# Optimization experiments

Measured on AMD Instinct MI355X. Metric: run time of the kernel, lower is better.

## Reference

```python
import jax, jax.numpy as jnp
import numpy as np
import math

N_EMBD = 2048
N_HEAD = 16
HEAD_DIM = N_EMBD // N_HEAD
EPS = 1e-6

def rms_norm(x, w):
    xf = x.astype(jnp.float32)
    n = xf * jax.lax.rsqrt(jnp.mean(xf * xf, axis=-1, keepdims=True) + EPS)
    return n.astype(x.dtype) * w

def rotate_embeddings(x):
    # pairs (a, b) -> (-b, a), interleaved on last dim
    x2 = x.reshape(*x.shape[:-1], -1, 2)
    rot = jnp.stack([-x2[..., 1], x2[..., 0]], axis=-1)
    return rot.reshape(x.shape)

def rope_angles(T, hd, dtype):
    # pos = 10000 ** ((-2*arange(0, hd, 2) - 1) / hd)  (faithful to source)
    i = jnp.arange(0, hd, 2, dtype=jnp.float32)
    pos = jnp.power(10000.0, (-2.0 * i - 1.0) / hd)
    token_seq = jnp.arange(T, dtype=jnp.float32)[:, None] * pos[None, :]  # [T, hd/2]
    ang = jnp.concatenate([token_seq, token_seq], axis=-1)  # [T, hd]
    return ang.astype(dtype)

def setup_inputs() -> dict:
    key = jax.random.key(0)
    k1, k2, k3 = jax.random.split(key, 3)
    B, T, C = 2, 2048, N_EMBD
    x = jax.random.normal(k1, (B, T, C), dtype=jnp.float32)
    s = 1.0 / math.sqrt(C)
    W_qkv = jax.random.normal(k2, (3 * C, C), dtype=jnp.float32) * s
    W_proj = jax.random.normal(k3, (C, C), dtype=jnp.float32) * s
    g_qk = jnp.ones((C,), dtype=jnp.float32)
    return {"x": x, "W_qkv": W_qkv, "W_proj": W_proj, "g_qk": g_qk}

def reference(x, W_qkv, W_proj, g_qk):
    B, T, C = x.shape
    H, hd = N_HEAD, HEAD_DIM
    qkv = x @ W_qkv.T  # [B, T, 3C]
    q, k, v = jnp.split(qkv, 3, axis=-1)
    q = rms_norm(q, g_qk)
    k = rms_norm(k, g_qk)
    # [B, H, T, hd]
    q = q.reshape(B, T, H, hd).transpose(0, 2, 1, 3)
    k = k.reshape(B, T, H, hd).transpose(0, 2, 1, 3)
    v = v.reshape(B, T, H, hd).transpose(0, 2, 1, 3)
    ang = rope_angles(T, hd, x.dtype)  # [T, hd]
    cos, sin = jnp.cos(ang), jnp.sin(ang)
    q = q * cos + rotate_embeddings(q) * sin
    k = k * cos + rotate_embeddings(k) * sin
    scale = 1.0 / math.sqrt(hd)  # muP = False
    att = jnp.einsum('bhqd,bhkd->bhqk', q, k) * scale
    causal = jnp.tril(jnp.ones((T, T), dtype=bool))
    att = jnp.where(causal, att, -jnp.inf)
    att = jax.nn.softmax(att, axis=-1)
    y = jnp.einsum('bhqk,bhkd->bhqd', att, v)
    y = y.transpose(0, 2, 1, 3).reshape(B, T, C)
    return y @ W_proj.T
```

## Files before the change

kernel.cpp:

```cpp
#include <hip/hip_runtime.h>
#include <math.h>

typedef __bf16 bf16x8 __attribute__((ext_vector_type(8)));
typedef float f32x4 __attribute__((ext_vector_type(4)));

__device__ __forceinline__ unsigned short f2bf(float x) {
  unsigned int u = __builtin_bit_cast(unsigned int, x);
  unsigned int r = (u + 0x7fffu + ((u >> 16) & 1u)) >> 16;
  return (unsigned short)r;
}
__device__ __forceinline__ float bf2f(unsigned short u) {
  return __builtin_bit_cast(float, ((unsigned int)u) << 16);
}
__device__ __forceinline__ void async16(const void* g, void* l) {
  __builtin_amdgcn_global_load_lds(
      (const __attribute__((address_space(1))) void*)g,
      (__attribute__((address_space(3))) void*)l, 16, 0, 0);
}

__global__ __launch_bounds__(256) void cvt_bf16_k(const float* __restrict__ in,
                                                  unsigned short* __restrict__ out,
                                                  int n8) {
  const int i = blockIdx.x * 256 + threadIdx.x;
  if (i >= n8) return;
  const float4* p = (const float4*)in + (long)i * 2;
  const float4 v0 = p[0], v1 = p[1];
  alignas(16) unsigned short o[8] = {f2bf(v0.x), f2bf(v0.y), f2bf(v0.z), f2bf(v0.w),
                                     f2bf(v1.x), f2bf(v1.y), f2bf(v1.z), f2bf(v1.w)};
  *(uint4*)(out + (long)i * 8) = *(uint4*)o;
}

__global__ __launch_bounds__(256) void rope_tab(float2* __restrict__ tab) {
  const int id = blockIdx.x * 256 + threadIdx.x;
  const int t = id >> 6, i = id & 63;
  const float kf = 13.287712379549449f / 128.f;
  const float a = (float)t * exp2f(-(4.f * (float)i + 1.f) * kf);
  float s, c;
  sincosf(a, &s, &c);
  tab[id] = make_float2(c, s);
}

template <int MODE>
__global__ __launch_bounds__(256) void gemm_bf(
    const unsigned short* __restrict__ A, const unsigned short* __restrict__ B,
    void* __restrict__ Cp, unsigned short* __restrict__ Vt, int M, int N, int K) {
  __shared__ unsigned short As[2][128 * 32];
  __shared__ unsigned short Bs[2][128 * 32];
  const int tid = threadIdx.x;
  const int lane = tid & 63;
  const int w = tid >> 6;
  const int wr = w >> 1, wc = w & 1;
  const int fr = lane & 15, fq = lane >> 4;
  const int nbx = gridDim.x;
  const int nwg = nbx * (int)gridDim.y;
  int bid = (int)blockIdx.y * nbx + (int)blockIdx.x;
  bid = (bid & 7) * (nwg >> 3) + (bid >> 3);
  const long m0 = (long)(bid / nbx) * 128;
  const long n0 = (long)(bid % nbx) * 128;
  const int sr = lane >> 2, sc = (lane & 3) * 8;
  f32x4 acc[4][4] = {};
  auto stage = [&](int buf, int k0) {
#pragma unroll
    for (int i = 0; i < 2; i++) {
      const int r = (w * 2 + i) * 16 + sr;
      async16(A + (m0 + r) * (long)K + k0 + sc, &As[buf][(w * 2 + i) * 512]);
      async16(B + (n0 + r) * (long)K + k0 + sc, &Bs[buf][(w * 2 + i) * 512]);
    }
  };
  int cur = 0;
  stage(0, 0);
  for (int k0 = 0; k0 < K; k0 += 32) {
    if (k0 + 32 < K) {
      stage(cur ^ 1, k0 + 32);
      asm volatile("s_waitcnt vmcnt(4)" ::: "memory");
    } else {
      asm volatile("s_waitcnt vmcnt(0)" ::: "memory");
    }
    __builtin_amdgcn_s_barrier();
    asm volatile("" ::: "memory");
    bf16x8 a[4], b[4];
#pragma unroll
    for (int i = 0; i < 4; i++)
      a[i] = *(const bf16x8*)&As[cur][(wr * 64 + i * 16 + fr) * 32 + fq * 8];
#pragma unroll
    for (int j = 0; j < 4; j++)
      b[j] = *(const bf16x8*)&Bs[cur][(wc * 64 + j * 16 + fr) * 32 + fq * 8];
#pragma unroll
    for (int i = 0; i < 4; i++)
#pragma unroll
      for (int j = 0; j < 4; j++)
        acc[i][j] =
            __builtin_amdgcn_mfma_f32_16x16x32_bf16(a[i], b[j], acc[i][j], 0, 0, 0);
    asm volatile("" ::: "memory");
    __builtin_amdgcn_s_barrier();
    asm volatile("" ::: "memory");
    cur ^= 1;
  }
  if (MODE == 0) {
    float* C = (float*)Cp;
#pragma unroll
    for (int i = 0; i < 4; i++)
#pragma unroll
      for (int j = 0; j < 4; j++)
#pragma unroll
        for (int r = 0; r < 4; r++) {
          const long m = m0 + wr * 64 + i * 16 + fq * 4 + r;
          const long n = n0 + wc * 64 + j * 16 + fr;
          C[m * N + n] = acc[i][j][r];
        }
  } else if (n0 < 4096) {
    unsigned short* C = (unsigned short*)Cp;
#pragma unroll
    for (int i = 0; i < 4; i++)
#pragma unroll
      for (int j = 0; j < 4; j++)
#pragma unroll
        for (int r = 0; r < 4; r++) {
          const long m = m0 + wr * 64 + i * 16 + fq * 4 + r;
          const long n = n0 + wc * 64 + j * 16 + fr;
          C[m * 4096 + n] = f2bf(acc[i][j][r]);
        }
  } else {
    const long vb = ((m0 >> 11) * 16 + ((n0 - 4096) >> 7)) * (128L * 2048);
#pragma unroll
    for (int i = 0; i < 4; i++)
#pragma unroll
      for (int j = 0; j < 4; j++) {
        const int d = wc * 64 + j * 16 + fr;
        const int t = (int)(m0 & 2047) + wr * 64 + i * 16 + fq * 4;
        alignas(8) unsigned short o[4] = {f2bf(acc[i][j][0]), f2bf(acc[i][j][1]),
                                          f2bf(acc[i][j][2]), f2bf(acc[i][j][3])};
        *(uint2*)&Vt[vb + (long)d * 2048 + t] = *(uint2*)o;
      }
  }
}

__global__ __launch_bounds__(256) void rms_rope(unsigned short* __restrict__ qkv,
                                                const float* __restrict__ g,
                                                const float2* __restrict__ tab) {
  const int m = blockIdx.x;
  const int t = m & 2047;
  const int tid = threadIdx.x;
  const int lane = tid & 63, w = tid >> 6;
  unsigned short* row = qkv + (long)m * 4096;
  const int base = tid * 8;
  alignas(16) unsigned short qs[8], ks[8];
  *(uint4*)qs = *(const uint4*)(row + base);
  *(uint4*)ks = *(const uint4*)(row + 2048 + base);
  float qv[8], kv[8];
  float sq = 0.f, sk = 0.f;
#pragma unroll
  for (int j = 0; j < 8; j++) {
    qv[j] = bf2f(qs[j]);
    kv[j] = bf2f(ks[j]);
    sq += qv[j] * qv[j];
    sk += kv[j] * kv[j];
  }
#pragma unroll
  for (int off = 1; off < 64; off <<= 1) {
    sq += __shfl_xor(sq, off);
    sk += __shfl_xor(sk, off);
  }
  __shared__ float red[2][4];
  if (lane == 0) {
    red[0][w] = sq;
    red[1][w] = sk;
  }
  __syncthreads();
  sq = red[0][0] + red[0][1] + red[0][2] + red[0][3];
  sk = red[1][0] + red[1][1] + red[1][2] + red[1][3];
  const float rq = rsqrtf(sq * (1.f / 2048.f) + 1e-6f);
  const float rk = rsqrtf(sk * (1.f / 2048.f) + 1e-6f);
  float qn[8], kn[8];
#pragma unroll
  for (int j = 0; j < 8; j++) {
    const float gg = g[base + j];
    qn[j] = qv[j] * rq * gg;
    kn[j] = kv[j] * rk * gg;
  }
  const float2* tp = tab + t * 64 + (base & 63);
  alignas(16) unsigned short qo[8], ko[8];
#pragma unroll
  for (int p = 0; p < 8; p += 2) {
    const float2 cs0 = tp[p];
    const float2 cs1 = tp[p + 1];
    qo[p] = f2bf(qn[p] * cs0.x - qn[p + 1] * cs0.y);
    qo[p + 1] = f2bf(qn[p + 1] * cs1.x + qn[p] * cs1.y);
    ko[p] = f2bf(kn[p] * cs0.x - kn[p + 1] * cs0.y);
    ko[p + 1] = f2bf(kn[p + 1] * cs1.x + kn[p] * cs1.y);
  }
  *(uint4*)(row + base) = *(uint4*)qo;
  *(uint4*)(row + 2048 + base) = *(uint4*)ko;
}

__global__ __launch_bounds__(256, 2) void attn64(
    const unsigned short* __restrict__ QKV, const unsigned short* __restrict__ VT,
    unsigned short* __restrict__ Y) {
  const int bid = blockIdx.x;
  const int r_ = bid & 7, s_ = bid >> 3;
  const int slot = s_ >> 5, j = s_ & 31;
  const int bh = r_ * 4 + slot;
  const int qt = (slot & 1) ? (31 - j) : j;
  const int b = bh >> 4, h = bh & 15;
  const int tid = threadIdx.x, lane = tid & 63, w = tid >> 6;
  const int fr = lane & 15, fq = lane >> 4;
  __shared__ unsigned short Kl[2][64 * 128];
  __shared__ unsigned short Vl[2][128 * 64];
  __shared__ unsigned short Pl[4][16 * 64];
  char* Pb = (char*)&Pl[w][0];
  const long tokbase = (long)b * 2048;
  const unsigned short* Qp = QKV + tokbase * 4096 + h * 128;
  const unsigned short* Kp = Qp + 2048;
  const unsigned short* Vg = VT + (long)bh * (128 * 2048);
  const int qbase = qt * 64;
  bf16x8 aq[4];
  {
    const unsigned short* qp = Qp + (long)(qbase + w * 16 + fr) * 4096 + fq * 8;
#pragma unroll
    for (int ks = 0; ks < 4; ks++) aq[ks] = *(const bf16x8*)(qp + ks * 32);
  }
  const int lH = lane >> 4, lL = (lane & 15) * 8;
  const int vH = lane >> 3, vL = (lane & 7) * 8;
  auto stage = [&](unsigned short* Kd, unsigned short* Vd, int kt) {
#pragma unroll
    for (int i = 0; i < 4; i++) {
      const int rowK = w * 4 + i * 16 + lH;
      async16(Kp + (long)(kt * 64 + rowK) * 4096 + (lL ^ ((rowK & 7) << 3)),
              Kd + w * 512 + i * 2048);
      const int rowV = w * 8 + i * 32 + vH;
      async16(Vg + (long)rowV * 2048 + kt * 64 + (vL ^ ((rowV & 7) << 3)),
              Vd + w * 512 + i * 2048);
    }
  };
  float m_i[4], l_i[4];
#pragma unroll
  for (int r = 0; r < 4; r++) {
    m_i[r] = -1e30f;
    l_i[r] = 0.f;
  }
  f32x4 accO[8] = {};
  const float scale = 0.08838834764831845f;
  int cur = 0;
  stage(Kl[0], Vl[0], 0);
  for (int kt = 0; kt <= qt; kt++) {
    if (kt < qt) {
      stage(Kl[cur ^ 1], Vl[cur ^ 1], kt + 1);
      asm volatile("s_waitcnt vmcnt(8)" ::: "memory");
    } else {
      asm volatile("s_waitcnt vmcnt(0)" ::: "memory");
    }
    __builtin_amdgcn_s_barrier();
    asm volatile("" ::: "memory");
    const unsigned short* Kc = Kl[cur];
    const unsigned short* Vc = Vl[cur];
    f32x4 accS[4] = {};
#pragma unroll
    for (int n = 0; n < 4; n++) {
      const int rowK = n * 16 + fr;
#pragma unroll
      for (int ks = 0; ks < 4; ks++) {
        bf16x8 bk =
            *(const bf16x8*)&Kc[rowK * 128 + ((ks * 32 + fq * 8) ^ ((fr & 7) << 3))];
        accS[n] = __builtin_amdgcn_mfma_f32_16x16x32_bf16(aq[ks], bk, accS[n], 0, 0, 0);
      }
    }
    if (kt == qt) {
#pragma unroll
      for (int n = 0; n < 4; n++)
#pragma unroll
        for (int r = 0; r < 4; r++) {
          const int key = kt * 64 + n * 16 + fr;
          const int qq = qbase + w * 16 + fq * 4 + r;
          accS[n][r] = (key > qq) ? -1e30f : accS[n][r] * scale;
        }
    } else {
#pragma unroll
      for (int n = 0; n < 4; n++)
#pragma unroll
        for (int r = 0; r < 4; r++) accS[n][r] *= scale;
    }
    float mx[4];
    bool need = false;
#pragma unroll
    for (int r = 0; r < 4; r++) {
      float m = fmaxf(fmaxf(accS[0][r], accS[1][r]), fmaxf(accS[2][r], accS[3][r]));
#pragma unroll
      for (int off = 1; off < 16; off <<= 1) m = fmaxf(m, __shfl_xor(m, off));
      mx[r] = m;
      need |= (m > m_i[r] + 8.f);
    }
    if (__any(need)) {
#pragma unroll
      for (int r = 0; r < 4; r++) {
        const float mnew = fmaxf(m_i[r], mx[r]);
        const float alpha = __expf(m_i[r] - mnew);
        m_i[r] = mnew;
        l_i[r] *= alpha;
#pragma unroll
        for (int ds = 0; ds < 8; ds++) accO[ds][r] *= alpha;
      }
    }
#pragma unroll
    for (int n = 0; n < 4; n++)
#pragma unroll
      for (int r = 0; r < 4; r++) accS[n][r] = __expf(accS[n][r] - m_i[r]);
#pragma unroll
    for (int r = 0; r < 4; r++) {
      float sum = accS[0][r] + accS[1][r] + accS[2][r] + accS[3][r];
#pragma unroll
      for (int off = 1; off < 16; off <<= 1) sum += __shfl_xor(sum, off);
      l_i[r] += sum;
    }
#pragma unroll
    for (int n = 0; n < 4; n++)
#pragma unroll
      for (int r = 0; r < 4; r++) {
        const int row = fq * 4 + r;
        const int byte = row * 128 + ((n * 32 + fr * 2) ^ ((row & 7) << 4));
        *(unsigned short*)(Pb + byte) = f2bf(accS[n][r]);
      }
#pragma unroll
    for (int ks = 0; ks < 2; ks++) {
      bf16x8 ap =
          *(const bf16x8*)(Pb + fr * 128 + ((ks * 64 + fq * 16) ^ ((fr & 7) << 4)));
#pragma unroll
      for (int ds = 0; ds < 8; ds++) {
        bf16x8 bv = *(const bf16x8*)&Vc[(ds * 16 + fr) * 64 +
                                        ((ks * 32 + fq * 8) ^ ((fr & 7) << 3))];
        accO[ds] = __builtin_amdgcn_mfma_f32_16x16x32_bf16(ap, bv, accO[ds], 0, 0, 0);
      }
    }
    asm volatile("" ::: "memory");
    __builtin_amdgcn_s_barrier();
    asm volatile("" ::: "memory");
    cur ^= 1;
  }
#pragma unroll
  for (int r = 0; r < 4; r++) l_i[r] = 1.f / l_i[r];
#pragma unroll
  for (int ds = 0; ds < 8; ds++)
#pragma unroll
    for (int r = 0; r < 4; r++) {
      const long trow = tokbase + qbase + w * 16 + fq * 4 + r;
      Y[trow * 2048 + h * 128 + ds * 16 + fr] = f2bf(accO[ds][r] * l_i[r]);
    }
}

extern "C" void kernel_launch(void* const* d_in, const int* in_sizes, int n_in,
                              void* d_out, int out_size, void* d_ws, size_t ws_size,
                              hipStream_t stream) {
  (void)out_size;
  (void)ws_size;
  const float *x = 0, *Wq = 0, *Wp = 0, *g = 0;
  for (int i = 0; i < n_in; i++) {
    switch (in_sizes[i]) {
      case 8388608: x = (const float*)d_in[i]; break;
      case 12582912: Wq = (const float*)d_in[i]; break;
      case 4194304: Wp = (const float*)d_in[i]; break;
      case 2048: g = (const float*)d_in[i]; break;
    }
  }
  if (!x) x = (const float*)d_in[0];
  if (!Wq) Wq = (const float*)d_in[1];
  if (!Wp) Wp = (const float*)d_in[2];
  if (!g) g = (const float*)d_in[3];
  float* out = (float*)d_out;
  char* ws = (char*)d_ws;
  unsigned short* qkv16 = (unsigned short*)ws;
  unsigned short* VtG = (unsigned short*)(ws + 33554432);
  unsigned short* Y = (unsigned short*)(ws + 50331648);
  unsigned short* xb = Y;
  unsigned short* Wqb = (unsigned short*)(ws + 67108864);
  unsigned short* Wpb = (unsigned short*)(ws + 92274688);
  float2* tab = (float2*)(ws + 100663296);

  cvt_bf16_k<<<4096, 256, 0, stream>>>(x, xb, 1048576);
  cvt_bf16_k<<<6144, 256, 0, stream>>>(Wq, Wqb, 1572864);
  cvt_bf16_k<<<2048, 256, 0, stream>>>(Wp, Wpb, 524288);
  rope_tab<<<512, 256, 0, stream>>>(tab);
  gemm_bf<1><<<dim3(48, 32), 256, 0, stream>>>(xb, Wqb, qkv16, VtG, 4096, 6144,
                                               2048);
  rms_rope<<<4096, 256, 0, stream>>>(qkv16, g, tab);
  attn64<<<1024, 256, 0, stream>>>(qkv16, VtG, Y);
  gemm_bf<0><<<dim3(16, 32), 256, 0, stream>>>(Y, Wpb, out, nullptr, 4096, 2048,
                                               2048);
}
```

Before: 424.9 us.

## Triple-buffer GEMM loads and widen attention to 128-query tiles with 8 waves

The GEMM's shared-memory pipeline goes from double to triple buffering, so loads are issued two K-steps ahead. The attention kernel now uses 512-thread blocks that each cover 128 queries over 64-key tiles, which shares each K/V tile across twice as many waves. It also replaces the per-wave diagonal mask with a per-wave row test, moves the row-sum shuffle reduction out of the inner loop to the end, and raises MFMA priority with s_setprio. The attention kernel asks for 4 blocks of 512 threads per CU, which adds register and LDS pressure, and the GEMM triple buffering raises its LDS use.

New measurement: 426.4 us. Within noise of the previous version (+0.3%).

```diff
diff --git a/kernel.cpp b/kernel.cpp
--- a/kernel.cpp
+++ b/kernel.cpp
@@ -44,8 +44,8 @@
 __global__ __launch_bounds__(256) void gemm_bf(
     const unsigned short* __restrict__ A, const unsigned short* __restrict__ B,
     void* __restrict__ Cp, unsigned short* __restrict__ Vt, int M, int N, int K) {
-  __shared__ unsigned short As[2][128 * 32];
-  __shared__ unsigned short Bs[2][128 * 32];
+  __shared__ unsigned short As[3][128 * 32];
+  __shared__ unsigned short Bs[3][128 * 32];
   const int tid = threadIdx.x;
   const int lane = tid & 63;
   const int w = tid >> 6;
@@ -69,9 +69,13 @@
   };
   int cur = 0;
   stage(0, 0);
+  stage(1, 32);
   for (int k0 = 0; k0 < K; k0 += 32) {
-    if (k0 + 32 < K) {
-      stage(cur ^ 1, k0 + 32);
+    if (k0 + 64 < K) {
+      const int nb = cur >= 1 ? cur - 1 : 2;
+      stage(nb, k0 + 64);
+      asm volatile("s_waitcnt vmcnt(8)" ::: "memory");
+    } else if (k0 + 32 < K) {
       asm volatile("s_waitcnt vmcnt(4)" ::: "memory");
     } else {
       asm volatile("s_waitcnt vmcnt(0)" ::: "memory");
@@ -94,7 +98,7 @@
     asm volatile("" ::: "memory");
     __builtin_amdgcn_s_barrier();
     asm volatile("" ::: "memory");
-    cur ^= 1;
+    cur = cur == 2 ? 0 : cur + 1;
   }
   if (MODE == 0) {
     float* C = (float*)Cp;
@@ -193,43 +197,43 @@
   *(uint4*)(row + 2048 + base) = *(uint4*)ko;
 }
 
-__global__ __launch_bounds__(256, 2) void attn64(
+__global__ __launch_bounds__(512, 4) void attn64(
     const unsigned short* __restrict__ QKV, const unsigned short* __restrict__ VT,
     unsigned short* __restrict__ Y) {
   const int bid = blockIdx.x;
   const int r_ = bid & 7, s_ = bid >> 3;
-  const int slot = s_ >> 5, j = s_ & 31;
+  const int slot = s_ >> 4, jj = s_ & 15;
   const int bh = r_ * 4 + slot;
-  const int qt = (slot & 1) ? (31 - j) : j;
+  const int qt = (jj & 1) ? 15 - (jj >> 1) : (jj >> 1);
   const int b = bh >> 4, h = bh & 15;
   const int tid = threadIdx.x, lane = tid & 63, w = tid >> 6;
   const int fr = lane & 15, fq = lane >> 4;
   __shared__ unsigned short Kl[2][64 * 128];
   __shared__ unsigned short Vl[2][128 * 64];
-  __shared__ unsigned short Pl[4][16 * 64];
+  __shared__ unsigned short Pl[8][16 * 64];
   char* Pb = (char*)&Pl[w][0];
   const long tokbase = (long)b * 2048;
   const unsigned short* Qp = QKV + tokbase * 4096 + h * 128;
   const unsigned short* Kp = Qp + 2048;
   const unsigned short* Vg = VT + (long)bh * (128 * 2048);
-  const int qbase = qt * 64;
+  const int qbase = qt * 128;
   bf16x8 aq[4];
   {
     const unsigned short* qp = Qp + (long)(qbase + w * 16 + fr) * 4096 + fq * 8;
 #pragma unroll
     for (int ks = 0; ks < 4; ks++) aq[ks] = *(const bf16x8*)(qp + ks * 32);
   }
-  const int lH = lane >> 4, lL = (lane & 15) * 8;
-  const int vH = lane >> 3, vL = (lane & 7) * 8;
+  const int kR = tid >> 4, kC = (tid & 15) * 8;
+  const int vR = tid >> 3, vC = (tid & 7) * 8;
   auto stage = [&](unsigned short* Kd, unsigned short* Vd, int kt) {
 #pragma unroll
-    for (int i = 0; i < 4; i++) {
-      const int rowK = w * 4 + i * 16 + lH;
-      async16(Kp + (long)(kt * 64 + rowK) * 4096 + (lL ^ ((rowK & 7) << 3)),
-              Kd + w * 512 + i * 2048);
-      const int rowV = w * 8 + i * 32 + vH;
-      async16(Vg + (long)rowV * 2048 + kt * 64 + (vL ^ ((rowV & 7) << 3)),
-              Vd + w * 512 + i * 2048);
+    for (int i = 0; i < 2; i++) {
+      const int rowK = i * 32 + kR;
+      async16(Kp + (long)(kt * 64 + rowK) * 4096 + (kC ^ ((rowK & 7) << 3)),
+              Kd + i * 4096 + tid * 8);
+      const int rowV = i * 64 + vR;
+      async16(Vg + (long)rowV * 2048 + kt * 64 + (vC ^ ((rowV & 7) << 3)),
+              Vd + i * 4096 + tid * 8);
     }
   };
   float m_i[4], l_i[4];
@@ -240,12 +244,13 @@
   }
   f32x4 accO[8] = {};
   const float scale = 0.08838834764831845f;
+  const int ktmax = 2 * qt + 1;
   int cur = 0;
   stage(Kl[0], Vl[0], 0);
-  for (int kt = 0; kt <= qt; kt++) {
-    if (kt < qt) {
+  for (int kt = 0; kt <= ktmax; kt++) {
+    if (kt < ktmax) {
       stage(Kl[cur ^ 1], Vl[cur ^ 1], kt + 1);
-      asm volatile("s_waitcnt vmcnt(8)" ::: "memory");
+      asm volatile("s_waitcnt vmcnt(4)" ::: "memory");
     } else {
       asm volatile("s_waitcnt vmcnt(0)" ::: "memory");
     }
@@ -254,6 +259,7 @@
     const unsigned short* Kc = Kl[cur];
     const unsigned short* Vc = Vl[cur];
     f32x4 accS[4] = {};
+    __builtin_amdgcn_s_setprio(1);
 #pragma unroll
     for (int n = 0; n < 4; n++) {
       const int rowK = n * 16 + fr;
@@ -264,7 +270,8 @@
         accS[n] = __builtin_amdgcn_mfma_f32_16x16x32_bf16(aq[ks], bk, accS[n], 0, 0, 0);
       }
     }
-    if (kt == qt) {
+    __builtin_amdgcn_s_setprio(0);
+    if (kt * 64 + 63 > qbase + w * 16) {
 #pragma unroll
       for (int n = 0; n < 4; n++)
 #pragma unroll
@@ -305,12 +312,8 @@
 #pragma unroll
       for (int r = 0; r < 4; r++) accS[n][r] = __expf(accS[n][r] - m_i[r]);
 #pragma unroll
-    for (int r = 0; r < 4; r++) {
-      float sum = accS[0][r] + accS[1][r] + accS[2][r] + accS[3][r];
-#pragma unroll
-      for (int off = 1; off < 16; off <<= 1) sum += __shfl_xor(sum, off);
-      l_i[r] += sum;
-    }
+    for (int r = 0; r < 4; r++)
+      l_i[r] += accS[0][r] + accS[1][r] + accS[2][r] + accS[3][r];
 #pragma unroll
     for (int n = 0; n < 4; n++)
 #pragma unroll
@@ -319,6 +322,7 @@
         const int byte = row * 128 + ((n * 32 + fr * 2) ^ ((row & 7) << 4));
         *(unsigned short*)(Pb + byte) = f2bf(accS[n][r]);
       }
+    __builtin_amdgcn_s_setprio(1);
 #pragma unroll
     for (int ks = 0; ks < 2; ks++) {
       bf16x8 ap =
@@ -330,13 +334,18 @@
         accO[ds] = __builtin_amdgcn_mfma_f32_16x16x32_bf16(ap, bv, accO[ds], 0, 0, 0);
       }
     }
+    __builtin_amdgcn_s_setprio(0);
     asm volatile("" ::: "memory");
     __builtin_amdgcn_s_barrier();
     asm volatile("" ::: "memory");
     cur ^= 1;
   }
 #pragma unroll
-  for (int r = 0; r < 4; r++) l_i[r] = 1.f / l_i[r];
+  for (int r = 0; r < 4; r++) {
+#pragma unroll
+    for (int off = 1; off < 16; off <<= 1) l_i[r] += __shfl_xor(l_i[r], off);
+    l_i[r] = 1.f / l_i[r];
+  }
 #pragma unroll
   for (int ds = 0; ds < 8; ds++)
 #pragma unroll
@@ -381,7 +390,7 @@
   gemm_bf<1><<<dim3(48, 32), 256, 0, stream>>>(xb, Wqb, qkv16, VtG, 4096, 6144,
                                                2048);
   rms_rope<<<4096, 256, 0, stream>>>(qkv16, g, tab);
-  attn64<<<1024, 256, 0, stream>>>(qkv16, VtG, Y);
+  attn64<<<512, 512, 0, stream>>>(qkv16, VtG, Y);
   gemm_bf<0><<<dim3(16, 32), 256, 0, stream>>>(Y, Wpb, out, nullptr, 4096, 2048,
                                                2048);
 }
```
